# Kernel tuning notes

Measured on AMD Instinct MI355X. Metric: run time of the kernel, lower is better.

Reference implementation:

```python
import jax, jax.numpy as jnp
import numpy as np

K = 2          # hops
N_HEAD = 34    # relation types
H = 100        # hidden size
BS = 32
N_NODE = 200
EPS = 1e-20
INIT_RANGE = 0.01


def setup_inputs() -> dict:
    key = jax.random.key(0)
    ks = jax.random.split(key, 7)
    X = jax.random.normal(ks[0], (BS, N_NODE, H), dtype=jnp.float32)
    A = (jax.random.uniform(ks[1], (BS, N_HEAD, N_NODE, N_NODE)) < 0.05).astype(jnp.float32)
    start_attn = jax.random.uniform(ks[2], (BS, N_NODE), dtype=jnp.float32)
    end_attn = jax.random.uniform(ks[3], (BS, N_NODE), dtype=jnp.float32)
    uni_attn = jax.random.uniform(ks[4], (BS, N_HEAD), dtype=jnp.float32)
    trans_attn = jax.random.uniform(ks[5], (BS, N_HEAD, N_HEAD), dtype=jnp.float32)
    # dense branch: diag_decompose=False, n_basis=0 -> (k, n_head+1, h, h)
    w_vs = jax.random.uniform(ks[6], (K, N_HEAD + 1, H, H), dtype=jnp.float32,
                              minval=-INIT_RANGE, maxval=INIT_RANGE)
    return dict(X=X, A=A, start_attn=start_attn, end_attn=end_attn,
                uni_attn=uni_attn, trans_attn=trans_attn, w_vs=w_vs)


def reference(X, A, start_attn, end_attn, uni_attn, trans_attn, w_vs):
    # _get_weights (n_basis == 0, diag_decompose == False)
    W = w_vs[:, :-1]   # (k, n_head, h, h)
    Wi = w_vs[:, -1]   # (k, h, h)
    W_pad = [jnp.eye(H, dtype=X.dtype)]
    for t in range(K - 1):
        W_pad = [Wi[K - 1 - t] @ W_pad[0]] + W_pad   # length k

    # ---- Z propagation ----
    Z0 = X * start_attn[:, :, None]                  # (b, n, h)
    Z_all = []
    Zprev = None                                     # (b, f, n, h) after a hop
    for t in range(K):
        if t == 0:
            Zin = jnp.broadcast_to(Z0[:, :, :, None], (BS, N_NODE, H, N_HEAD))
        else:
            # permute + bmm with trans_attn: mix over incoming head f -> g
            Zin = jnp.einsum('bfni,bfg->bnig', Zprev, trans_attn)
        # per-head feature transform: (b,n,i,f) x (f,i,o) -> (b,f,n,o)
        Zh = jnp.einsum('bnif,fio->bfno', Zin, W[t])
        Zh = Zh * uni_attn[:, :, None, None]
        # adjacency propagation per head: A (b,f,m,n) x Z (b,f,n,o)
        Zh = jnp.einsum('bfmn,bfno->bfmo', A, Zh)    # (b, f, n, h)
        # sum heads, project with W_pad[t], gate by end_attn
        Zt = jnp.einsum('bfno,oi->bni', Zh, W_pad[t])
        Zt = Zt * end_attn[:, :, None]
        Z_all.append(Zt)
        Zprev = Zh

    # ---- degree normalizer D ----
    D_all = []
    Dprev = None                                     # (b, f, n)
    for t in range(K):
        if t == 0:
            Din = jnp.broadcast_to(start_attn[:, None, :], (BS, N_HEAD, N_NODE))
        else:
            Din = jnp.einsum('bfn,bfg->bgn', Dprev, trans_attn)
        Dh = Din * uni_attn[:, :, None]
        Dh = jnp.einsum('bfmn,bfn->bfm', A, Dh)      # (b, f, n)
        D_all.append(Dh.sum(axis=1) * end_attn)
        Dprev = Dh

    # per-hop outputs, normalized; stacked as (k, b, n, h)
    out = jnp.stack([Z / (D[:, :, None] + EPS) for Z, D in zip(Z_all, D_all)])
    return out
```

## Files before the change

kernel.cpp:

```cpp
#include <hip/hip_runtime.h>
#include <hip/hip_bf16.h>

#define NHEAD 34
#define HDIM  100
#define NNODE 200
#define NBATCH 32
#define EPSV 1e-20f

typedef __attribute__((ext_vector_type(8))) short bf16x8;
typedef __attribute__((ext_vector_type(4))) float f32x4;
typedef __attribute__((ext_vector_type(16))) float f32x16;
typedef __attribute__((ext_vector_type(4))) unsigned int ux4;

__device__ inline unsigned short bf16rne(float x) {
    return __bfloat16_as_ushort(__float2bfloat16(x));
}
__device__ inline float bf16tof(unsigned short h) {
    unsigned u = ((unsigned)h) << 16;
    return __builtin_bit_cast(float, u);
}

__device__ inline void split3_8(const float* v, bf16x8& p0, bf16x8& p1, bf16x8& p2) {
    #pragma unroll
    for (int j = 0; j < 8; j++) {
        float x = v[j];
        unsigned short h0 = bf16rne(x); float r1 = x - bf16tof(h0);
        unsigned short h1 = bf16rne(r1); float r2 = r1 - bf16tof(h1);
        unsigned short h2 = bf16rne(r2);
        p0[j] = (short)h0; p1[j] = (short)h1; p2[j] = (short)h2;
    }
}

__device__ inline void split2s(float x, unsigned short& h0, unsigned short& h1) {
    h0 = bf16rne(x);
    h1 = bf16rne(x - bf16tof(h0));
}
__device__ inline void split2_pack8(const float* v, bf16x8& a0, bf16x8& a1) {
    #pragma unroll
    for (int j = 0; j < 8; j++) {
        unsigned short h0, h1; split2s(v[j], h0, h1);
        a0[j] = (short)h0; a1[j] = (short)h1;
    }
}

__device__ inline bf16x8 afrag_bits(unsigned byte) {
    ux4 p;
    #pragma unroll
    for (int r = 0; r < 4; r++) {
        p[r] = ((byte >> (2 * r)) & 1u) * 0x3F80u + ((byte >> (2 * r + 1)) & 1u) * 0x3F800000u;
    }
    return __builtin_bit_cast(bf16x8, p);
}

__global__ __launch_bounds__(1024) void a_bitmask(const float* __restrict__ A,
                                                  unsigned long long* __restrict__ bm) {
    int row = blockIdx.x * 16 + (threadIdx.x >> 6);
    int lane = threadIdx.x & 63;
    if (row >= NBATCH * NHEAD * NNODE) return;
    const float* Ar = A + (size_t)row * NNODE;
    unsigned long long w0 = __ballot(Ar[lane] != 0.0f);
    unsigned long long w1 = __ballot(Ar[64 + lane] != 0.0f);
    unsigned long long w2 = __ballot(Ar[128 + lane] != 0.0f);
    unsigned long long w3 = __ballot(lane < 8 ? (Ar[192 + lane] != 0.0f) : false);
    if (lane == 0) {
        unsigned long long* p = bm + (size_t)row * 4;
        p[0] = w0; p[1] = w1; p[2] = w2; p[3] = w3;
    }
}

__global__ __launch_bounds__(256) void wsplit(const float* __restrict__ wv,
                                              short* __restrict__ wfr) {
    int fw = blockIdx.x;
    const float* W = wv + (size_t)(fw / 34) * 350000 + (size_t)(fw % 34) * 10000;
    for (int s0 = threadIdx.x; s0 < 28 * 64; s0 += 256) {
        int frag = s0 >> 6;
        int l = s0 & 63;
        int nt = frag >> 2, ks = frag & 3;
        int n = nt * 16 + (l & 15);
        int kb = ks * 32 + ((l >> 4) << 3);
        float v[8];
        #pragma unroll
        for (int j = 0; j < 8; j++) {
            int k = kb + j;
            v[j] = (k < 100 && n < 100) ? W[k * 100 + n] : 0.0f;
        }
        bf16x8 p0, p1, p2;
        split3_8(v, p0, p1, p2);
        size_t base = (((size_t)fw * 28 + frag) * 3) * 512 + l * 8;
        *(bf16x8*)&wfr[base]        = p0;
        *(bf16x8*)&wfr[base + 512]  = p1;
        *(bf16x8*)&wfr[base + 1024] = p2;
    }
}

__global__ __launch_bounds__(256) void asplit(const float* __restrict__ X,
                                              const float* __restrict__ start,
                                              short* __restrict__ xfr) {
    int b = blockIdx.x;
    const float* Xb = X + (size_t)b * 20000;
    const float* st = start + (size_t)b * NNODE;
    for (int s0 = threadIdx.x; s0 < 52 * 64; s0 += 256) {
        int frag = s0 >> 6;
        int l = s0 & 63;
        int mt = frag >> 2, ks = frag & 3;
        int row = mt * 16 + (l & 15);
        int kb = ks * 32 + ((l >> 4) << 3);
        float sc = (row < 200) ? st[row] : 0.0f;
        float v[8];
        #pragma unroll
        for (int j = 0; j < 8; j++) {
            int k = kb + j;
            v[j] = (row < 200 && k < 100) ? Xb[row * 100 + k] * sc : 0.0f;
        }
        bf16x8 p0, p1, p2;
        split3_8(v, p0, p1, p2);
        size_t base = (((size_t)b * 52 + frag) * 3) * 512 + l * 8;
        *(bf16x8*)&xfr[base]        = p0;
        *(bf16x8*)&xfr[base + 512]  = p1;
        *(bf16x8*)&xfr[base + 1024] = p2;
    }
}

template <int T>
__global__ __launch_bounds__(1024, 8) void fused_zha(
    const unsigned* __restrict__ bm32,
    const short* __restrict__ xfr,
    const float* __restrict__ Sfp,
    const short* __restrict__ wfr_t,
    const float* __restrict__ uni,
    const float* __restrict__ start,
    const float* __restrict__ dvec_g,
    float* __restrict__ Zout, float* __restrict__ Dh)
{
    int g = blockIdx.y * 68 + blockIdx.x;
    int wk = (g & 7) * 272 + (g >> 3);
    int b = wk / 68;
    int rem = wk - b * 68;
    int f = rem >> 1, ch = rem & 1;
    size_t bf = (size_t)b * NHEAD + f;
    int tid = threadIdx.x;
    int l = tid & 63, w = tid >> 6;

    __shared__ __align__(16) short zpl[2][64][216];
    __shared__ unsigned mkl[8][225];

    const unsigned* bmw = bm32 + bf * 1600;
    for (int idx = tid; idx < 1600; idx += 1024) mkl[idx & 7][idx >> 3] = bmw[idx];
    if (tid < 200) mkl[tid / 25][200 + tid % 25] = 0u;

    float u = uni[b * NHEAD + f];

    if (ch == 1) {
        if (tid < 200) {
            float dv;
            if constexpr (T == 0) dv = start[b * NNODE + tid] * u;
            else                  dv = dvec_g[bf * NNODE + tid];
            unsigned short h0, h1; split2s(dv, h0, h1);
            zpl[0][36][tid] = (short)h0; zpl[1][36][tid] = (short)h1;
        } else if (tid < 232) {
            int r = 200 + ((tid - 200) & 15), s = (tid - 200) >> 4;
            zpl[s][36][r] = 0;
        }
    }

    const short* WF = wfr_t + (size_t)f * 28 * 3 * 512;
    int ntb = ch ? 4 : 0, nte = ch ? 7 : 4;
    int coff = ch * 64;
    for (int mt = w; mt < 13; mt += 16) {
        bf16x8 A0[4], A1[4];
        if constexpr (T == 0) {
            const short* AG = xfr + ((size_t)b * 52 + mt * 4) * 3 * 512;
            #pragma unroll
            for (int ks = 0; ks < 4; ks++) {
                A0[ks] = *(const bf16x8*)&AG[(ks * 3 + 0) * 512 + l * 8];
                A1[ks] = *(const bf16x8*)&AG[(ks * 3 + 1) * 512 + l * 8];
            }
        } else {
            const float* S = Sfp + bf * 20000;
            int row = mt * 16 + (l & 15);
            bool rok = row < 200;
            #pragma unroll
            for (int ks = 0; ks < 4; ks++) {
                int kb = ks * 32 + ((l >> 4) << 3);
                float4 z4 = make_float4(0.f, 0.f, 0.f, 0.f);
                float4 v0 = (rok && kb < 100)     ? *(const float4*)&S[row * 100 + kb]     : z4;
                float4 v1 = (rok && kb + 4 < 100) ? *(const float4*)&S[row * 100 + kb + 4] : z4;
                float vv[8] = {v0.x, v0.y, v0.z, v0.w, v1.x, v1.y, v1.z, v1.w};
                split2_pack8(vv, A0[ks], A1[ks]);
            }
        }
        for (int nt = ntb; nt < nte; nt++) {
            f32x4 acc = {0.f, 0.f, 0.f, 0.f};
            #pragma unroll
            for (int ks = 0; ks < 4; ks++) {
                const short* wp = &WF[(size_t)((nt * 4 + ks) * 3) * 512 + l * 8];
                bf16x8 B0 = *(const bf16x8*)&wp[0];
                bf16x8 B1 = *(const bf16x8*)&wp[512];
                acc = __builtin_amdgcn_mfma_f32_16x16x32_bf16(A0[ks], B0, acc, 0, 0, 0);
                acc = __builtin_amdgcn_mfma_f32_16x16x32_bf16(A1[ks], B0, acc, 0, 0, 0);
                acc = __builtin_amdgcn_mfma_f32_16x16x32_bf16(A0[ks], B1, acc, 0, 0, 0);
            }
            int c = nt * 16 + (l & 15);
            if (c < 100) {
                int nb = mt * 16 + ((l >> 4) << 2);
                short4 q0, q1;
                #pragma unroll
                for (int r = 0; r < 4; r++) {
                    unsigned short h0, h1; split2s(acc[r] * u, h0, h1);
                    ((short*)&q0)[r] = (short)h0;
                    ((short*)&q1)[r] = (short)h1;
                }
                *(short4*)&zpl[0][c - coff][nb] = q0;
                *(short4*)&zpl[1][c - coff][nb] = q1;
            }
        }
    }
    __syncthreads();

    int cl = l & 31, kg = l >> 5;
    int mt2 = w >> 1, cg = w & 1;
    int myl = cg * 32 + cl;
    bool act = (w < 14);

    f32x16 acc2;
    #pragma unroll
    for (int i = 0; i < 16; i++) acc2[i] = 0.f;

    if (act) {
        for (int ks = 0; ks < 13; ks++) {
            bf16x8 z0 = *(const bf16x8*)&zpl[0][myl][ks * 16 + kg * 8];
            bf16x8 z1 = *(const bf16x8*)&zpl[1][myl][ks * 16 + kg * 8];
            unsigned word = mkl[ks >> 1][mt2 * 32 + cl];
            unsigned byte = (word >> (((ks & 1) << 4) | (kg << 3))) & 0xFFu;
            bf16x8 af = afrag_bits(byte);
            acc2 = __builtin_amdgcn_mfma_f32_32x32x16_bf16(af, z0, acc2, 0, 0, 0);
            acc2 = __builtin_amdgcn_mfma_f32_32x32x16_bf16(af, z1, acc2, 0, 0, 0);
        }
    }
    __syncthreads();

    float* zs = (float*)&zpl[0][0][0];
    if (act) {
        int myg = coff + myl;
        if (myg <= 100) {
            #pragma unroll
            for (int r = 0; r < 16; r++) {
                int m = mt2 * 32 + (r & 3) + ((r >> 2) << 3) + (kg << 2);
                if (m < 200) zs[m * 68 + myl] = acc2[r];
            }
        }
    }
    __syncthreads();

    float* Zob = Zout + bf * 20000;
    if (ch == 0) {
        for (int idx = tid; idx < 3200; idx += 1024) {
            int m = idx >> 4, c4 = idx & 15;
            *(float4*)&Zob[m * 100 + c4 * 4] = *(const float4*)&zs[m * 68 + c4 * 4];
        }
    } else {
        float* Dhb = Dh + bf * NNODE;
        for (int idx = tid; idx < 2000; idx += 1024) {
            int m = idx / 10, c4 = idx % 10;
            if (c4 < 9) *(float4*)&Zob[m * 100 + 64 + c4 * 4] = *(const float4*)&zs[m * 68 + c4 * 4];
            else Dhb[m] = zs[m * 68 + 36];
        }
    }
}

__global__ __launch_bounds__(256) void out0_gemm(
    const float* __restrict__ src, const float* __restrict__ W,
    const float* __restrict__ rowscale, float* __restrict__ dst)
{
    int c = blockIdx.x, b = blockIdx.y;
    const float* S = src + (size_t)b * 20000;
    float* Dst = dst + (size_t)b * 20000;

    __shared__ __align__(16) float wl[10000];
    __shared__ __align__(16) float xl[5000];

    int tid = threadIdx.x;
    for (int idx = tid; idx < 10000; idx += 256) wl[idx] = W[idx];
    int base = c * 5000;
    for (int idx = tid; idx < 5000; idx += 256) xl[idx] = S[base + idx];
    __syncthreads();

    int q = tid % 25;
    int ty = tid / 25;
    if (ty < 10) {
        float4 acc[5];
        #pragma unroll
        for (int r = 0; r < 5; r++) acc[r] = make_float4(0.f, 0.f, 0.f, 0.f);
        #pragma unroll 2
        for (int i = 0; i < 100; i++) {
            float4 w4 = *(const float4*)&wl[i * 100 + q * 4];
            #pragma unroll
            for (int r = 0; r < 5; r++) {
                float x = xl[(ty + 10 * r) * 100 + i];
                acc[r].x += x * w4.x; acc[r].y += x * w4.y;
                acc[r].z += x * w4.z; acc[r].w += x * w4.w;
            }
        }
        #pragma unroll
        for (int r = 0; r < 5; r++) {
            int n = c * 50 + ty + 10 * r;
            float sc = rowscale[b * NNODE + n];
            float4 o4 = make_float4(acc[r].x * sc, acc[r].y * sc, acc[r].z * sc, acc[r].w * sc);
            *(float4*)&Dst[n * 100 + q * 4] = o4;
        }
    }
}

__global__ void dmix_rs(const float* __restrict__ Dh0, const float* __restrict__ trans,
                        const float* __restrict__ uni, const float* __restrict__ endat,
                        float* __restrict__ dvec1, float* __restrict__ rs0) {
    int b = blockIdx.x;
    __shared__ float tl[NHEAD * NHEAD];
    for (int idx = threadIdx.x; idx < NHEAD * NHEAD; idx += 256) tl[idx] = trans[b * NHEAD * NHEAD + idx];
    __syncthreads();
    int n = threadIdx.x;
    if (n < NNODE) {
        float dh[NHEAD];
        float s = 0.f;
        #pragma unroll
        for (int f = 0; f < NHEAD; f++) { dh[f] = Dh0[((size_t)b * NHEAD + f) * NNODE + n]; s += dh[f]; }
        float e = endat[b * NNODE + n];
        rs0[b * NNODE + n] = e / (e * s + EPSV);
        #pragma unroll
        for (int g = 0; g < NHEAD; g++) {
            float acc = 0.f;
            #pragma unroll
            for (int f = 0; f < NHEAD; f++) acc += dh[f] * tl[f * NHEAD + g];
            dvec1[((size_t)b * NHEAD + g) * NNODE + n] = uni[b * NHEAD + g] * acc;
        }
    }
}

__global__ void dsum_rs(const float* __restrict__ Dh, const float* __restrict__ endat,
                        float* __restrict__ rs) {
    int idx = blockIdx.x * 256 + threadIdx.x;
    if (idx >= NBATCH * NNODE) return;
    int b = idx / NNODE, m = idx % NNODE;
    float s = 0.f;
    #pragma unroll
    for (int f = 0; f < NHEAD; f++) s += Dh[((size_t)b * NHEAD + f) * NNODE + m];
    float e = endat[idx];
    rs[idx] = e / (e * s + EPSV);
}

__global__ __launch_bounds__(256) void hmix(
    const float* __restrict__ Zsrc, const float* __restrict__ trans,
    float* __restrict__ Zdst, float* __restrict__ Zsum)
{
    int b = blockIdx.y;
    int c2 = blockIdx.x * 256 + threadIdx.x;
    __shared__ __align__(8) float tl[NHEAD * NHEAD];
    for (int idx = threadIdx.x; idx < NHEAD * NHEAD; idx += 256) tl[idx] = trans[b * NHEAD * NHEAD + idx];
    __syncthreads();
    if (c2 >= 10000) return;
    const float2* Zb = (const float2*)(Zsrc + (size_t)b * NHEAD * 20000) + c2;
    float2 acc[NHEAD];
    #pragma unroll
    for (int g = 0; g < NHEAD; g++) acc[g] = make_float2(0.f, 0.f);
    float2 s = make_float2(0.f, 0.f);
    for (int f = 0; f < NHEAD; f++) {
        float2 vf = Zb[(size_t)f * 10000];
        s.x += vf.x; s.y += vf.y;
        const float2* row = (const float2*)&tl[f * NHEAD];
        #pragma unroll
        for (int gq = 0; gq < 17; gq++) {
            float2 t2 = row[gq];
            acc[2 * gq].x     += vf.x * t2.x; acc[2 * gq].y     += vf.y * t2.x;
            acc[2 * gq + 1].x += vf.x * t2.y; acc[2 * gq + 1].y += vf.y * t2.y;
        }
    }
    ((float2*)(Zsum + (size_t)b * 20000))[c2] = s;
    float2* Zd = (float2*)(Zdst + (size_t)b * NHEAD * 20000) + c2;
    #pragma unroll
    for (int g = 0; g < NHEAD; g++) Zd[(size_t)g * 10000] = acc[g];
}

__global__ void fsum_out(const float* __restrict__ Zacc, const float* __restrict__ rs,
                         float* __restrict__ out) {
    int idx = blockIdx.x * 256 + threadIdx.x;
    if (idx >= NBATCH * 10000) return;
    int b = idx / 10000;
    int c2 = idx % 10000;
    const float2* Zb = (const float2*)(Zacc + (size_t)b * NHEAD * 20000) + c2;
    float2 s = make_float2(0.f, 0.f);
    #pragma unroll
    for (int g = 0; g < NHEAD; g++) {
        float2 v = Zb[(size_t)g * 10000];
        s.x += v.x; s.y += v.y;
    }
    int n = (c2 * 2) / 100;
    float r = rs[b * NNODE + n];
    s.x *= r; s.y *= r;
    ((float2*)out)[idx] = s;
}

extern "C" void kernel_launch(void* const* d_in, const int* in_sizes, int n_in,
                              void* d_out, int out_size, void* d_ws, size_t ws_size,
                              hipStream_t stream) {
    (void)in_sizes; (void)n_in;
    const float* X     = (const float*)d_in[0];
    const float* A     = (const float*)d_in[1];
    const float* start = (const float*)d_in[2];
    const float* endat = (const float*)d_in[3];
    const float* uni   = (const float*)d_in[4];
    const float* trans = (const float*)d_in[5];
    const float* wv    = (const float*)d_in[6];
    float* out = (float*)d_out;
    float* ws  = (float*)d_ws;

    size_t off = 0;
    unsigned long long* bm = (unsigned long long*)(ws); off += 1740800;
    float* buf1  = ws + off; off += 21760000;
    float* buf2  = ws + off; off += 21760000;
    float* Dh0   = ws + off; off += 217600;
    float* dvec1 = ws + off; off += 217600;
    float* Dh1   = ws + off; off += 217600;
    float* rs0   = ws + off; off += 6400;
    float* rs1   = ws + off; off += 6400;
    float* Zsum0 = ws + off; off += 640000;
    short* wfr   = (short*)(ws + off); off += 1462272;
    short* xfr   = (short*)(ws + off); off += 1277952;
    if (ws_size < off * sizeof(float)) {
        hipMemsetAsync(d_out, 0x7F, (size_t)out_size * sizeof(float), stream);
        return;
    }

    const float* Wi1 = wv + 690000;
    const short* wfr0 = wfr;
    const short* wfr1 = wfr + (size_t)34 * 28 * 3 * 512;
    const unsigned* bm32 = (const unsigned*)bm;

    dim3 gBF(NHEAD * 2, NBATCH);

    a_bitmask<<<(NBATCH * NHEAD * NNODE + 15) / 16, 1024, 0, stream>>>(A, bm);
    wsplit<<<68, 256, 0, stream>>>(wv, wfr);
    asplit<<<32, 256, 0, stream>>>(X, start, xfr);

    fused_zha<0><<<gBF, 1024, 0, stream>>>(bm32, xfr, nullptr, wfr0, uni, start, nullptr, buf2, Dh0);
    dmix_rs<<<NBATCH, 256, 0, stream>>>(Dh0, trans, uni, endat, dvec1, rs0);
    hmix<<<dim3(40, NBATCH), 256, 0, stream>>>(buf2, trans, buf1, Zsum0);
    out0_gemm<<<dim3(4, NBATCH), 256, 0, stream>>>(Zsum0, Wi1, rs0, out);

    fused_zha<1><<<gBF, 1024, 0, stream>>>(bm32, nullptr, buf1, wfr1, uni, nullptr, dvec1, buf2, Dh1);
    dsum_rs<<<(NBATCH * NNODE + 255) / 256, 256, 0, stream>>>(Dh1, endat, rs1);
    fsum_out<<<(NBATCH * 10000 + 255) / 256, 256, 0, stream>>>(buf2, rs1, out + 640000);
}
```

Before: 332.2 us.

## Fuse adjacency bitmask build into first hop kernel, store two-part bf16 splits

Drops the separate a_bitmask pass and has the first-hop fused kernel read the float adjacency directly, ballot it into the shared-memory mask, and write the global bitmask (only from the ch==0 block) for reuse in hop two. The weight and input fragment buffers now hold two bf16 parts instead of three, since the third part was never read. This saves a kernel launch and a separate pass of mask writes and reads, at the cost of both channel blocks reading the full A slice. It relies on the hop-two kernel running after hop one so the bitmask is already written.

```diff
diff --git a/kernel.cpp b/kernel.cpp
--- a/kernel.cpp
+++ b/kernel.cpp
@@ -20,17 +20,6 @@
     return __builtin_bit_cast(float, u);
 }
 
-__device__ inline void split3_8(const float* v, bf16x8& p0, bf16x8& p1, bf16x8& p2) {
-    #pragma unroll
-    for (int j = 0; j < 8; j++) {
-        float x = v[j];
-        unsigned short h0 = bf16rne(x); float r1 = x - bf16tof(h0);
-        unsigned short h1 = bf16rne(r1); float r2 = r1 - bf16tof(h1);
-        unsigned short h2 = bf16rne(r2);
-        p0[j] = (short)h0; p1[j] = (short)h1; p2[j] = (short)h2;
-    }
-}
-
 __device__ inline void split2s(float x, unsigned short& h0, unsigned short& h1) {
     h0 = bf16rne(x);
     h1 = bf16rne(x - bf16tof(h0));
@@ -50,22 +39,6 @@
         p[r] = ((byte >> (2 * r)) & 1u) * 0x3F80u + ((byte >> (2 * r + 1)) & 1u) * 0x3F800000u;
     }
     return __builtin_bit_cast(bf16x8, p);
-}
-
-__global__ __launch_bounds__(1024) void a_bitmask(const float* __restrict__ A,
-                                                  unsigned long long* __restrict__ bm) {
-    int row = blockIdx.x * 16 + (threadIdx.x >> 6);
-    int lane = threadIdx.x & 63;
-    if (row >= NBATCH * NHEAD * NNODE) return;
-    const float* Ar = A + (size_t)row * NNODE;
-    unsigned long long w0 = __ballot(Ar[lane] != 0.0f);
-    unsigned long long w1 = __ballot(Ar[64 + lane] != 0.0f);
-    unsigned long long w2 = __ballot(Ar[128 + lane] != 0.0f);
-    unsigned long long w3 = __ballot(lane < 8 ? (Ar[192 + lane] != 0.0f) : false);
-    if (lane == 0) {
-        unsigned long long* p = bm + (size_t)row * 4;
-        p[0] = w0; p[1] = w1; p[2] = w2; p[3] = w3;
-    }
 }
 
 __global__ __launch_bounds__(256) void wsplit(const float* __restrict__ wv,
@@ -84,12 +57,11 @@
             int k = kb + j;
             v[j] = (k < 100 && n < 100) ? W[k * 100 + n] : 0.0f;
         }
-        bf16x8 p0, p1, p2;
-        split3_8(v, p0, p1, p2);
-        size_t base = (((size_t)fw * 28 + frag) * 3) * 512 + l * 8;
-        *(bf16x8*)&wfr[base]        = p0;
-        *(bf16x8*)&wfr[base + 512]  = p1;
-        *(bf16x8*)&wfr[base + 1024] = p2;
+        bf16x8 p0, p1;
+        split2_pack8(v, p0, p1);
+        size_t base = (((size_t)fw * 28 + frag) * 2) * 512 + l * 8;
+        *(bf16x8*)&wfr[base]       = p0;
+        *(bf16x8*)&wfr[base + 512] = p1;
     }
 }
 
@@ -112,18 +84,17 @@
             int k = kb + j;
             v[j] = (row < 200 && k < 100) ? Xb[row * 100 + k] * sc : 0.0f;
         }
-        bf16x8 p0, p1, p2;
-        split3_8(v, p0, p1, p2);
-        size_t base = (((size_t)b * 52 + frag) * 3) * 512 + l * 8;
-        *(bf16x8*)&xfr[base]        = p0;
-        *(bf16x8*)&xfr[base + 512]  = p1;
-        *(bf16x8*)&xfr[base + 1024] = p2;
+        bf16x8 p0, p1;
+        split2_pack8(v, p0, p1);
+        size_t base = (((size_t)b * 52 + frag) * 2) * 512 + l * 8;
+        *(bf16x8*)&xfr[base]       = p0;
+        *(bf16x8*)&xfr[base + 512] = p1;
     }
 }
 
 template <int T>
 __global__ __launch_bounds__(1024, 8) void fused_zha(
-    const unsigned* __restrict__ bm32,
+    unsigned* __restrict__ bm32,
     const short* __restrict__ xfr,
     const float* __restrict__ Sfp,
     const short* __restrict__ wfr_t,
@@ -144,8 +115,29 @@
     __shared__ __align__(16) short zpl[2][64][216];
     __shared__ unsigned mkl[8][225];
 
-    const unsigned* bmw = bm32 + bf * 1600;
-    for (int idx = tid; idx < 1600; idx += 1024) mkl[idx & 7][idx >> 3] = bmw[idx];
+    if constexpr (T == 0) {
+        const float* Ab = Sfp + bf * 40000;
+        for (int m = w; m < 200; m += 16) {
+            const float* Ar = Ab + m * 200;
+            unsigned long long b0 = __ballot(Ar[l] != 0.0f);
+            unsigned long long b1 = __ballot(Ar[64 + l] != 0.0f);
+            unsigned long long b2 = __ballot(Ar[128 + l] != 0.0f);
+            unsigned long long b3 = __ballot(l < 8 ? (Ar[192 + l] != 0.0f) : false);
+            if (l == 0) {
+                mkl[0][m] = (unsigned)b0; mkl[1][m] = (unsigned)(b0 >> 32);
+                mkl[2][m] = (unsigned)b1; mkl[3][m] = (unsigned)(b1 >> 32);
+                mkl[4][m] = (unsigned)b2; mkl[5][m] = (unsigned)(b2 >> 32);
+                mkl[6][m] = (unsigned)b3; mkl[7][m] = (unsigned)(b3 >> 32);
+                if (ch == 0) {
+                    unsigned long long* p = (unsigned long long*)bm32 + ((size_t)bf * 200 + m) * 4;
+                    p[0] = b0; p[1] = b1; p[2] = b2; p[3] = b3;
+                }
+            }
+        }
+    } else {
+        const unsigned* bmw = bm32 + bf * 1600;
+        for (int idx = tid; idx < 1600; idx += 1024) mkl[idx & 7][idx >> 3] = bmw[idx];
+    }
     if (tid < 200) mkl[tid / 25][200 + tid % 25] = 0u;
 
     float u = uni[b * NHEAD + f];
@@ -163,17 +155,17 @@
         }
     }
 
-    const short* WF = wfr_t + (size_t)f * 28 * 3 * 512;
+    const short* WF = wfr_t + (size_t)f * 28 * 2 * 512;
     int ntb = ch ? 4 : 0, nte = ch ? 7 : 4;
     int coff = ch * 64;
     for (int mt = w; mt < 13; mt += 16) {
         bf16x8 A0[4], A1[4];
         if constexpr (T == 0) {
-            const short* AG = xfr + ((size_t)b * 52 + mt * 4) * 3 * 512;
+            const short* AG = xfr + ((size_t)b * 52 + mt * 4) * 2 * 512;
             #pragma unroll
             for (int ks = 0; ks < 4; ks++) {
-                A0[ks] = *(const bf16x8*)&AG[(ks * 3 + 0) * 512 + l * 8];
-                A1[ks] = *(const bf16x8*)&AG[(ks * 3 + 1) * 512 + l * 8];
+                A0[ks] = *(const bf16x8*)&AG[(ks * 2 + 0) * 512 + l * 8];
+                A1[ks] = *(const bf16x8*)&AG[(ks * 2 + 1) * 512 + l * 8];
             }
         } else {
             const float* S = Sfp + bf * 20000;
@@ -193,7 +185,7 @@
             f32x4 acc = {0.f, 0.f, 0.f, 0.f};
             #pragma unroll
             for (int ks = 0; ks < 4; ks++) {
-                const short* wp = &WF[(size_t)((nt * 4 + ks) * 3) * 512 + l * 8];
+                const short* wp = &WF[(size_t)((nt * 4 + ks) * 2) * 512 + l * 8];
                 bf16x8 B0 = *(const bf16x8*)&wp[0];
                 bf16x8 B1 = *(const bf16x8*)&wp[512];
                 acc = __builtin_amdgcn_mfma_f32_16x16x32_bf16(A0[ks], B0, acc, 0, 0, 0);
@@ -414,7 +406,7 @@
     float* ws  = (float*)d_ws;
 
     size_t off = 0;
-    unsigned long long* bm = (unsigned long long*)(ws); off += 1740800;
+    unsigned* bm32 = (unsigned*)(ws); off += 1740800;
     float* buf1  = ws + off; off += 21760000;
     float* buf2  = ws + off; off += 21760000;
     float* Dh0   = ws + off; off += 217600;
@@ -423,8 +415,8 @@
     float* rs0   = ws + off; off += 6400;
     float* rs1   = ws + off; off += 6400;
     float* Zsum0 = ws + off; off += 640000;
-    short* wfr   = (short*)(ws + off); off += 1462272;
-    short* xfr   = (short*)(ws + off); off += 1277952;
+    short* wfr   = (short*)(ws + off); off += 974848;
+    short* xfr   = (short*)(ws + off); off += 851968;
     if (ws_size < off * sizeof(float)) {
         hipMemsetAsync(d_out, 0x7F, (size_t)out_size * sizeof(float), stream);
         return;
@@ -432,16 +424,14 @@
 
     const float* Wi1 = wv + 690000;
     const short* wfr0 = wfr;
-    const short* wfr1 = wfr + (size_t)34 * 28 * 3 * 512;
-    const unsigned* bm32 = (const unsigned*)bm;
+    const short* wfr1 = wfr + (size_t)34 * 28 * 2 * 512;
 
     dim3 gBF(NHEAD * 2, NBATCH);
 
-    a_bitmask<<<(NBATCH * NHEAD * NNODE + 15) / 16, 1024, 0, stream>>>(A, bm);
     wsplit<<<68, 256, 0, stream>>>(wv, wfr);
     asplit<<<32, 256, 0, stream>>>(X, start, xfr);
 
-    fused_zha<0><<<gBF, 1024, 0, stream>>>(bm32, xfr, nullptr, wfr0, uni, start, nullptr, buf2, Dh0);
+    fused_zha<0><<<gBF, 1024, 0, stream>>>(bm32, xfr, A, wfr0, uni, start, nullptr, buf2, Dh0);
     dmix_rs<<<NBATCH, 256, 0, stream>>>(Dh0, trans, uni, endat, dvec1, rs0);
     hmix<<<dim3(40, NBATCH), 256, 0, stream>>>(buf2, trans, buf1, Zsum0);
     out0_gemm<<<dim3(4, NBATCH), 256, 0, stream>>>(Zsum0, Wi1, rs0, out);
```

Result: slower. 364.3 us (+9.7%).
